# Kernel tuning notes

Measured on AMD Instinct MI355X. Metric: run time of the kernel, lower is better.

The kernel has to match this reference:

```python
import jax, jax.numpy as jnp
import numpy as np

D = 1024; H = 8; QLR = 384; KVLR = 256; NOPE = 128; ROPE = 64; VD = 128
E = 8; TOPK = 2; INTER = 512; NSH = 2; B = 2; T = 2048
QKD = NOPE + ROPE  # 192


def _rms(x, w, eps=1e-6):
    return x * jax.lax.rsqrt(jnp.mean(x * x, axis=-1, keepdims=True) + eps) * w


def _rope(x, cos, sin):
    # x: [B,T,h,ROPE]; pairs are consecutive elements (torch view(...,-1,2)).
    x0 = x[..., 0::2]
    x1 = x[..., 1::2]
    c = cos[None, :, None, :]
    s = sin[None, :, None, :]
    y0 = x0 * c - x1 * s
    y1 = x0 * s + x1 * c
    return jnp.stack([y0, y1], axis=-1).reshape(x.shape)


def setup_inputs() -> dict:
    key = jax.random.key(0)
    ks = jax.random.split(key, 12)
    def w(k, shape, scale=0.02):
        return jax.random.normal(k, shape, dtype=jnp.float32) * scale
    inv = 1.0 / (10000.0 ** (jnp.arange(0, ROPE, 2, dtype=jnp.float32) / ROPE))
    ang = jnp.arange(T, dtype=jnp.float32)[:, None] * inv[None, :]  # [T, ROPE//2]
    return {
        "x": jax.random.normal(ks[0], (B, T, D), dtype=jnp.float32),
        "freqs_cos": jnp.cos(ang),
        "freqs_sin": jnp.sin(ang),
        "rmsn1_w": jnp.ones((D,), jnp.float32),
        "rmsn2_w": jnp.ones((D,), jnp.float32),
        "latent_w": w(ks[1], (D, QLR + KVLR + ROPE)),
        "q_norm_w": jnp.ones((QLR,), jnp.float32),
        "q_up_w": w(ks[2], (QLR, H * QKD)),
        "kv_norm_w": jnp.ones((KVLR,), jnp.float32),
        "kv_up_w": w(ks[3], (KVLR, H * (NOPE + VD))),
        "c_proj_w": w(ks[4], (D, D)),
        "gate_w": w(ks[5], (D, E)),
        "sh_w1": w(ks[6], (D, INTER * NSH)),
        "sh_w2": w(ks[7], (INTER * NSH, D)),
        "sh_w3": w(ks[8], (D, INTER * NSH)),
        "e_w1": w(ks[9], (E, D, INTER)),
        "e_w2": w(ks[10], (E, INTER, D)),
        "e_w3": w(ks[11], (E, D, INTER)),
    }


def reference(x, freqs_cos, freqs_sin, rmsn1_w, rmsn2_w, latent_w, q_norm_w,
              q_up_w, kv_norm_w, kv_up_w, c_proj_w, gate_w, sh_w1, sh_w2,
              sh_w3, e_w1, e_w2, e_w3):
    Bx, Tx, _ = x.shape
    # ---- MLA attention ----
    h = _rms(x, rmsn1_w)
    lat = h @ latent_w
    q_l, kv_l, k_r = jnp.split(lat, [QLR, QLR + KVLR], axis=-1)
    q = (_rms(q_l, q_norm_w) @ q_up_w).reshape(Bx, Tx, H, QKD)
    q_n, q_r = q[..., :NOPE], q[..., NOPE:]
    q_r = _rope(q_r, freqs_cos, freqs_sin)
    q = jnp.concatenate([q_n, q_r], axis=-1)  # [B,T,H,QKD]
    kv = (_rms(kv_l, kv_norm_w) @ kv_up_w).reshape(Bx, Tx, H, NOPE + VD)
    k_n, v = kv[..., :NOPE], kv[..., NOPE:]
    k_r = _rope(k_r[:, :, None, :], freqs_cos, freqs_sin)
    k_r = jnp.broadcast_to(k_r, (Bx, Tx, H, ROPE))
    k = jnp.concatenate([k_n, k_r], axis=-1)
    scale = 1.0 / jnp.sqrt(jnp.float32(QKD))
    scores = jnp.einsum('bqhd,bkhd->bhqk', q, k) * scale
    causal = jnp.tril(jnp.ones((Tx, Tx), dtype=bool))
    scores = jnp.where(causal, scores, jnp.finfo(scores.dtype).min)
    attn = jax.nn.softmax(scores, axis=-1)
    y = jnp.einsum('bhqk,bkhd->bqhd', attn, v).reshape(Bx, Tx, D)
    x = x + y @ c_proj_w
    # ---- DeepSeekMoE ----
    h2 = _rms(x, rmsn2_w).reshape(-1, D)  # [N, D]
    y_sh = (jax.nn.silu(h2 @ sh_w1) * (h2 @ sh_w3)) @ sh_w2
    scores_g = jax.nn.softmax(h2 @ gate_w, axis=-1)  # [N, E]
    w_top, idx = jax.lax.top_k(scores_g, TOPK)  # weights == gathered original scores
    # combine weights per expert (route_scale = 1.0)
    cw = jnp.sum(jax.nn.one_hot(idx, E, dtype=h2.dtype) * w_top[..., None], axis=1)  # [N, E]
    h1 = jnp.einsum('nd,edi->eni', h2, e_w1)
    h3 = jnp.einsum('nd,edi->eni', h2, e_w3)
    out_e = jnp.einsum('eni,eid->end', jax.nn.silu(h1) * h3, e_w2)  # [E, N, D]
    y_moe = y_sh + jnp.einsum('end,ne->nd', out_e, cw)
    return x + y_moe.reshape(Bx, Tx, D)
```

## Files before the change

kernel.cpp:

```cpp
#include <hip/hip_runtime.h>
#include <hip/hip_bf16.h>
#include <math.h>

#define D_ 1024
#define H_ 8
#define QLR_ 384
#define KVLR_ 256
#define NOPE_ 128
#define ROPE_ 64
#define VD_ 128
#define E_ 8
#define INTER_ 512
#define B_ 2
#define T_ 2048
#define QKD_ 192
#define NTOK (B_*T_)
#define LSTR 4608
#define MAXMB 72

typedef __attribute__((ext_vector_type(8))) short short8;
typedef __attribute__((ext_vector_type(4))) float f32x4;
typedef __attribute__((ext_vector_type(4))) unsigned short us4;

__device__ __forceinline__ unsigned short f2bf(float f) {
  union { float f; unsigned u; } v; v.f = f;
  return (unsigned short)((v.u + 0x7FFFu + ((v.u >> 16) & 1u)) >> 16);
}
__device__ __forceinline__ float bf2f(unsigned short h) {
  union { unsigned u; float f; } v; v.u = ((unsigned)h) << 16;
  return v.f;
}

#define GLD16(SRC, DST) __builtin_amdgcn_global_load_lds( \
    (__attribute__((address_space(1))) void*)(SRC), \
    (__attribute__((address_space(3))) void*)(DST), 16, 0, 0)

#define DPPF(v, ctrl) __int_as_float(__builtin_amdgcn_update_dpp(0, __float_as_int(v), ctrl, 0xF, 0xF, true))
__device__ __forceinline__ float dppmax16(float v) {
  v = fmaxf(v, DPPF(v, 0xB1));
  v = fmaxf(v, DPPF(v, 0x4E));
  v = fmaxf(v, DPPF(v, 0x124));
  v = fmaxf(v, DPPF(v, 0x128));
  return v;
}
__device__ __forceinline__ float dppsum16(float v) {
  v += DPPF(v, 0xB1);
  v += DPPF(v, 0x4E);
  v += DPPF(v, 0x124);
  v += DPPF(v, 0x128);
  return v;
}

__global__ __launch_bounds__(256) void transpose_f32_bf16(
    const float* __restrict__ in, unsigned short* __restrict__ out,
    int R, int C, size_t inBS, size_t outBS) {
  __shared__ float tile[32][33];
  const float* inp = in + (size_t)blockIdx.z * inBS;
  unsigned short* outp = out + (size_t)blockIdx.z * outBS;
  int c0 = blockIdx.x * 32, r0 = blockIdx.y * 32;
  int tx = threadIdx.x & 31, ty = threadIdx.x >> 5;
  #pragma unroll
  for (int i = 0; i < 4; ++i) {
    int rr = ty + i * 8;
    tile[rr][tx] = inp[(size_t)(r0 + rr) * C + c0 + tx];
  }
  __syncthreads();
  #pragma unroll
  for (int i = 0; i < 4; ++i) {
    int rr = ty + i * 8;
    outp[(size_t)(c0 + rr) * R + r0 + tx] = f2bf(tile[tx][rr]);
  }
}

__global__ __launch_bounds__(256) void transpose_pair(
    const float* __restrict__ in1, const float* __restrict__ in3,
    unsigned short* __restrict__ out, int K, int C1, size_t inBS, size_t outBS) {
  __shared__ float tile[32][33];
  int z = blockIdx.z; int bat = z >> 1; int f = (z & 1) * 16;
  const float* src = ((z & 1) ? in3 : in1) + (size_t)bat * inBS;
  unsigned short* o = out + (size_t)bat * outBS;
  int c0 = blockIdx.x * 32, r0 = blockIdx.y * 32;
  int tx = threadIdx.x & 31, ty = threadIdx.x >> 5;
  #pragma unroll
  for (int i = 0; i < 4; ++i) {
    int rr = ty + i * 8;
    tile[rr][tx] = src[(size_t)(r0 + rr) * C1 + c0 + tx];
  }
  __syncthreads();
  #pragma unroll
  for (int i = 0; i < 4; ++i) {
    int cc = ty + i * 8;
    int c = c0 + cc;
    int n = ((c >> 4) << 5) + (c & 15) + f;
    o[(size_t)n * K + r0 + tx] = f2bf(tile[tx][cc]);
  }
}

template<typename TI>
__global__ __launch_bounds__(256) void rms_to_bf16(
    const TI* __restrict__ src, int stride, int off, const float* __restrict__ w,
    unsigned short* __restrict__ out, int Dd, int outStride) {
  int row = blockIdx.x;
  const TI* xr = src + (size_t)row * stride + off;
  float ss = 0.f;
  for (int i = threadIdx.x; i < Dd; i += 256) {
    float v;
    if constexpr (sizeof(TI) == 2) v = bf2f((unsigned short)xr[i]); else v = (float)xr[i];
    ss += v * v;
  }
  for (int o = 1; o < 64; o <<= 1) ss += __shfl_xor(ss, o);
  __shared__ float red[4];
  if ((threadIdx.x & 63) == 0) red[threadIdx.x >> 6] = ss;
  __syncthreads();
  float tot = red[0] + red[1] + red[2] + red[3];
  float inv = 1.f / sqrtf(tot / Dd + 1e-6f);
  for (int i = threadIdx.x; i < Dd; i += 256) {
    float v;
    if constexpr (sizeof(TI) == 2) v = bf2f((unsigned short)xr[i]); else v = (float)xr[i];
    out[(size_t)row * outStride + i] = f2bf(v * inv * w[i]);
  }
}

__global__ __launch_bounds__(256) void lat_post(
    const unsigned short* __restrict__ lat, const float* __restrict__ qw,
    const float* __restrict__ kw, const float* __restrict__ fc, const float* __restrict__ fs,
    unsigned short* __restrict__ qn, unsigned short* __restrict__ kvn,
    unsigned short* __restrict__ kr) {
  int row = blockIdx.x, tid = threadIdx.x;
  int lane = tid & 63, wv = tid >> 6;
  const unsigned short* lr = lat + (size_t)row * 768;
  float s1 = 0.f, s2 = 0.f;
  for (int i = tid; i < QLR_; i += 256) { float v = bf2f(lr[i]); s1 += v * v; }
  { float v = bf2f(lr[QLR_ + tid]); s2 = v * v; }
  for (int o = 1; o < 64; o <<= 1) { s1 += __shfl_xor(s1, o); s2 += __shfl_xor(s2, o); }
  __shared__ float red[8];
  if (lane == 0) { red[wv] = s1; red[4 + wv] = s2; }
  __syncthreads();
  float inv1 = 1.f / sqrtf((red[0] + red[1] + red[2] + red[3]) / QLR_ + 1e-6f);
  float inv2 = 1.f / sqrtf((red[4] + red[5] + red[6] + red[7]) / KVLR_ + 1e-6f);
  for (int i = tid; i < QLR_; i += 256)
    qn[(size_t)row * QLR_ + i] = f2bf(bf2f(lr[i]) * inv1 * qw[i]);
  kvn[(size_t)row * KVLR_ + tid] = f2bf(bf2f(lr[QLR_ + tid]) * inv2 * kw[tid]);
  if (tid < 32) {
    int t = row & (T_ - 1);
    float c = fc[t * 32 + tid], s = fs[t * 32 + tid];
    float x0 = bf2f(lr[640 + 2 * tid]), x1 = bf2f(lr[640 + 2 * tid + 1]);
    kr[(size_t)row * ROPE_ + 2 * tid]     = f2bf(x0 * c - x1 * s);
    kr[(size_t)row * ROPE_ + 2 * tid + 1] = f2bf(x0 * s + x1 * c);
  }
}

template<int MODE>
__global__ __launch_bounds__(256) void gemm_bf16(
    const unsigned short* __restrict__ A, const unsigned short* __restrict__ Bt,
    void* __restrict__ Cv, int M, int N, int K,
    const float* __restrict__ addv) {
  __shared__ __align__(16) unsigned short As[128 * 32];
  __shared__ __align__(16) unsigned short Bs[128 * 32];
  const int tid = threadIdx.x;
  const int lane = tid & 63, wave = tid >> 6;
  const int wm = wave >> 1, wn = wave & 1;
  const int bm = blockIdx.y * 128, bn = blockIdx.x * 128;
  const int r = lane & 15, g = lane >> 4;

  f32x4 acc[4][4];
  #pragma unroll
  for (int i = 0; i < 4; ++i)
    #pragma unroll
    for (int j = 0; j < 4; ++j) acc[i][j] = (f32x4)0.f;

  const int rl0 = wave * 16 + (lane >> 2);
  const int rl1 = rl0 + 64;
  const int kc = (lane & 3) * 8;
  char* AsB = (char*)As; char* BsB = (char*)Bs;

  for (int k0 = 0; k0 < K; k0 += 32) {
    GLD16(A + (size_t)(bm + rl0) * K + k0 + kc, AsB + wave * 1024);
    GLD16(A + (size_t)(bm + rl1) * K + k0 + kc, AsB + (wave + 4) * 1024);
    GLD16(Bt + (size_t)(bn + rl0) * K + k0 + kc, BsB + wave * 1024);
    GLD16(Bt + (size_t)(bn + rl1) * K + k0 + kc, BsB + (wave + 4) * 1024);
    __syncthreads();
    short8 af[4], bfr[4];
    #pragma unroll
    for (int mi = 0; mi < 4; ++mi)
      af[mi] = *(const short8*)(As + (wm * 64 + mi * 16 + r) * 32 + g * 8);
    #pragma unroll
    for (int nj = 0; nj < 4; ++nj)
      bfr[nj] = *(const short8*)(Bs + (wn * 64 + nj * 16 + r) * 32 + g * 8);
    #pragma unroll
    for (int mi = 0; mi < 4; ++mi)
      #pragma unroll
      for (int nj = 0; nj < 4; ++nj)
        acc[mi][nj] = __builtin_amdgcn_mfma_f32_16x16x32_bf16(af[mi], bfr[nj], acc[mi][nj], 0, 0, 0);
    __syncthreads();
  }

  const int orow0 = wm * 64 + g * 4;
  const int ocol0 = bn + wn * 64 + r;
  #pragma unroll
  for (int mi = 0; mi < 4; ++mi) {
    #pragma unroll
    for (int reg = 0; reg < 4; ++reg) {
      int mrow = bm + orow0 + mi * 16 + reg;
      size_t bas = (size_t)mrow * N + ocol0;
      if (MODE == 0) {
        unsigned short* C = (unsigned short*)Cv;
        #pragma unroll
        for (int nj = 0; nj < 4; ++nj) C[bas + nj * 16] = f2bf(acc[mi][nj][reg]);
      } else {
        float* C = (float*)Cv;
        #pragma unroll
        for (int nj = 0; nj < 4; ++nj) C[bas + nj * 16] = acc[mi][nj][reg] + addv[bas + nj * 16];
      }
    }
  }
}

__global__ __launch_bounds__(256) void gemm_qkv(
    const unsigned short* __restrict__ qn, const unsigned short* __restrict__ Wqup,
    const unsigned short* __restrict__ kvn, const unsigned short* __restrict__ Wkv,
    unsigned short* __restrict__ qq, unsigned short* __restrict__ kvb,
    unsigned short* __restrict__ vtg) {
  __shared__ __align__(16) unsigned short As[128 * 32];
  __shared__ __align__(16) unsigned short Bs[128 * 32];
  const int tid = threadIdx.x;
  const int lane = tid & 63, wave = tid >> 6;
  const int wm = wave >> 1, wn = wave & 1;
  const bool isQ = blockIdx.x < 12;
  const int bx = isQ ? blockIdx.x : blockIdx.x - 12;
  const unsigned short* A  = isQ ? qn : kvn;
  const unsigned short* Bt = isQ ? Wqup : Wkv;
  const int K = isQ ? QLR_ : KVLR_;
  const int bm = blockIdx.y * 128, bn = bx * 128;
  const int r = lane & 15, g = lane >> 4;

  f32x4 acc[4][4];
  #pragma unroll
  for (int i = 0; i < 4; ++i)
    #pragma unroll
    for (int j = 0; j < 4; ++j) acc[i][j] = (f32x4)0.f;

  const int rl0 = wave * 16 + (lane >> 2);
  const int rl1 = rl0 + 64;
  const int kc = (lane & 3) * 8;
  char* AsB = (char*)As; char* BsB = (char*)Bs;

  for (int k0 = 0; k0 < K; k0 += 32) {
    GLD16(A + (size_t)(bm + rl0) * K + k0 + kc, AsB + wave * 1024);
    GLD16(A + (size_t)(bm + rl1) * K + k0 + kc, AsB + (wave + 4) * 1024);
    GLD16(Bt + (size_t)(bn + rl0) * K + k0 + kc, BsB + wave * 1024);
    GLD16(Bt + (size_t)(bn + rl1) * K + k0 + kc, BsB + (wave + 4) * 1024);
    __syncthreads();
    short8 af[4], bfr[4];
    #pragma unroll
    for (int mi = 0; mi < 4; ++mi)
      af[mi] = *(const short8*)(As + (wm * 64 + mi * 16 + r) * 32 + g * 8);
    #pragma unroll
    for (int nj = 0; nj < 4; ++nj)
      bfr[nj] = *(const short8*)(Bs + (wn * 64 + nj * 16 + r) * 32 + g * 8);
    #pragma unroll
    for (int mi = 0; mi < 4; ++mi)
      #pragma unroll
      for (int nj = 0; nj < 4; ++nj)
        acc[mi][nj] = __builtin_amdgcn_mfma_f32_16x16x32_bf16(af[mi], bfr[nj], acc[mi][nj], 0, 0, 0);
    __syncthreads();
  }

  if (isQ) {
    const int orow0 = wm * 64 + g * 4;
    const int ocol0 = bn + wn * 64 + r;
    #pragma unroll
    for (int mi = 0; mi < 4; ++mi)
      #pragma unroll
      for (int reg = 0; reg < 4; ++reg) {
        int mrow = bm + orow0 + mi * 16 + reg;
        size_t bas = (size_t)mrow * 1536 + ocol0;
        #pragma unroll
        for (int nj = 0; nj < 4; ++nj) qq[bas + nj * 16] = f2bf(acc[mi][nj][reg]);
      }
  } else {
    const int colbase = bn + wn * 64;
    const int b = bm >> 11;
    const int hh = colbase >> 8;
    if ((colbase & 255) < 128) {
      #pragma unroll
      for (int mi = 0; mi < 4; ++mi)
        #pragma unroll
        for (int reg = 0; reg < 4; ++reg) {
          int mrow = bm + wm * 64 + mi * 16 + g * 4 + reg;
          size_t bas = (size_t)mrow * 2048 + colbase + r;
          #pragma unroll
          for (int nj = 0; nj < 4; ++nj) kvb[bas + nj * 16] = f2bf(acc[mi][nj][reg]);
        }
    } else {
      const int tl0 = (bm & 2047) + wm * 64 + g * 4;
      const int d0 = (colbase & 255) - 128 + r;
      const size_t bhbase = (size_t)(b * 8 + hh) * 64;
      #pragma unroll
      for (int mi = 0; mi < 4; ++mi) {
        int t = tl0 + mi * 16;
        size_t tb = (bhbase + (t >> 5)) * 4096 + (t & 31);
        #pragma unroll
        for (int nj = 0; nj < 4; ++nj) {
          int d = d0 + nj * 16;
          us4 pk;
          #pragma unroll
          for (int reg = 0; reg < 4; ++reg) pk[reg] = f2bf(acc[mi][nj][reg]);
          *(us4*)(vtg + tb + (size_t)d * 32) = pk;
        }
      }
    }
  }
}

__global__ __launch_bounds__(256) void gemm_ffn13(
    const unsigned short* __restrict__ h2b, const unsigned short* __restrict__ Wsh13,
    unsigned short* __restrict__ t1m,
    const unsigned short* __restrict__ Wew13, unsigned short* __restrict__ ehm,
    const int* __restrict__ lists, const int* __restrict__ map, const int* __restrict__ sbase) {
  __shared__ __align__(16) unsigned short As[128 * 32];
  __shared__ __align__(16) unsigned short Bs[128 * 32];
  const int i = blockIdx.x;
  const bool isSh = i < 512;
  const int tid = threadIdx.x, lane = tid & 63, wave = tid >> 6;
  const int wm = wave >> 1, wn = wave & 1;
  const int r = lane & 15, g = lane >> 4;
  const int rl0 = wave * 16 + (lane >> 2), rl1 = rl0 + 64;
  const int kc = (lane & 3) * 8;

  int bn, e = 0, ib = 0, bm = 0;
  const unsigned short* Bt;
  int ar0, ar1;
  const unsigned short* A;
  if (isSh) {
    bn = (i & 15) * 128; bm = (i >> 4) * 128;
    Bt = Wsh13; A = h2b;
    ar0 = bm + rl0; ar1 = bm + rl1;
  } else {
    int j = i - 512;
    bn = (j & 7) * 128;
    int mb = map[j >> 3];
    if (mb < 0) return;
    e = mb >> 16; ib = mb & 0xFFFF;
    Bt = Wew13 + (size_t)e * 1024 * 1024; A = h2b;
    ar0 = lists[e * LSTR + ib * 128 + rl0]; if (ar0 < 0) ar0 = 0;
    ar1 = lists[e * LSTR + ib * 128 + rl1]; if (ar1 < 0) ar1 = 0;
  }

  f32x4 acc[4][4];
  #pragma unroll
  for (int a = 0; a < 4; ++a)
    #pragma unroll
    for (int bj = 0; bj < 4; ++bj) acc[a][bj] = (f32x4)0.f;
  char* AsB = (char*)As; char* BsB = (char*)Bs;

  for (int k0 = 0; k0 < 1024; k0 += 32) {
    GLD16(A + (size_t)ar0 * 1024 + k0 + kc, AsB + wave * 1024);
    GLD16(A + (size_t)ar1 * 1024 + k0 + kc, AsB + (wave + 4) * 1024);
    GLD16(Bt + (size_t)(bn + rl0) * 1024 + k0 + kc, BsB + wave * 1024);
    GLD16(Bt + (size_t)(bn + rl1) * 1024 + k0 + kc, BsB + (wave + 4) * 1024);
    __syncthreads();
    short8 af[4], bfr[4];
    #pragma unroll
    for (int mi = 0; mi < 4; ++mi)
      af[mi] = *(const short8*)(As + (wm * 64 + mi * 16 + r) * 32 + g * 8);
    #pragma unroll
    for (int nj = 0; nj < 4; ++nj)
      bfr[nj] = *(const short8*)(Bs + (wn * 64 + nj * 16 + r) * 32 + g * 8);
    #pragma unroll
    for (int mi = 0; mi < 4; ++mi)
      #pragma unroll
      for (int nj = 0; nj < 4; ++nj)
        acc[mi][nj] = __builtin_amdgcn_mfma_f32_16x16x32_bf16(af[mi], bfr[nj], acc[mi][nj], 0, 0, 0);
    __syncthreads();
  }

  if (isSh) {
    const int hc = ((bn + wn * 64) >> 1) + r;
    #pragma unroll
    for (int mi = 0; mi < 4; ++mi)
      #pragma unroll
      for (int reg = 0; reg < 4; ++reg) {
        int mrow = bm + wm * 64 + mi * 16 + g * 4 + reg;
        #pragma unroll
        for (int p = 0; p < 2; ++p) {
          float a = acc[mi][2 * p][reg], b3 = acc[mi][2 * p + 1][reg];
          t1m[(size_t)mrow * 1024 + hc + p * 16] = f2bf((a / (1.f + __expf(-a))) * b3);
        }
      }
  } else {
    const int sb = sbase[e] + ib * 128;
    const int hc = ((bn + wn * 64) >> 1) + r;
    #pragma unroll
    for (int mi = 0; mi < 4; ++mi)
      #pragma unroll
      for (int reg = 0; reg < 4; ++reg) {
        int srow = sb + wm * 64 + mi * 16 + g * 4 + reg;
        #pragma unroll
        for (int p = 0; p < 2; ++p) {
          float a = acc[mi][2 * p][reg], b3 = acc[mi][2 * p + 1][reg];
          ehm[(size_t)srow * 512 + hc + p * 16] = f2bf((a / (1.f + __expf(-a))) * b3);
        }
      }
  }
}

__global__ __launch_bounds__(256) void gemm_ffn2(
    const unsigned short* __restrict__ t1m, const unsigned short* __restrict__ Wsh2,
    const unsigned short* __restrict__ ehm, const unsigned short* __restrict__ Wew2,
    float* __restrict__ out,
    const int* __restrict__ lists, const int* __restrict__ map, const int* __restrict__ sbase,
    const float* __restrict__ cw) {
  __shared__ __align__(16) unsigned short As[128 * 32];
  __shared__ __align__(16) unsigned short Bs[128 * 32];
  const int i = blockIdx.x;
  const bool isSh = i < 256;
  const int tid = threadIdx.x, lane = tid & 63, wave = tid >> 6;
  const int wm = wave >> 1, wn = wave & 1;
  const int r = lane & 15, g = lane >> 4;
  const int rl0 = wave * 16 + (lane >> 2), rl1 = rl0 + 64;
  const int kc = (lane & 3) * 8;

  int bn, e = 0, ib = 0, bm = 0, K;
  const unsigned short* A;
  const unsigned short* Bt;
  if (isSh) {
    bn = (i & 7) * 128; bm = (i >> 3) * 128;
    A = t1m; Bt = Wsh2; K = 1024;
  } else {
    int j = i - 256;
    bn = (j & 7) * 128;
    int mb = map[j >> 3];
    if (mb < 0) return;
    e = mb >> 16; ib = mb & 0xFFFF;
    bm = sbase[e] + ib * 128;
    A = ehm; Bt = Wew2 + (size_t)e * 512 * 1024; K = 512;
  }

  f32x4 acc[4][4];
  #pragma unroll
  for (int a = 0; a < 4; ++a)
    #pragma unroll
    for (int bj = 0; bj < 4; ++bj) acc[a][bj] = (f32x4)0.f;
  char* AsB = (char*)As; char* BsB = (char*)Bs;

  for (int k0 = 0; k0 < K; k0 += 32) {
    GLD16(A + (size_t)(bm + rl0) * K + k0 + kc, AsB + wave * 1024);
    GLD16(A + (size_t)(bm + rl1) * K + k0 + kc, AsB + (wave + 4) * 1024);
    GLD16(Bt + (size_t)(bn + rl0) * K + k0 + kc, BsB + wave * 1024);
    GLD16(Bt + (size_t)(bn + rl1) * K + k0 + kc, BsB + (wave + 4) * 1024);
    __syncthreads();
    short8 af[4], bfr[4];
    #pragma unroll
    for (int mi = 0; mi < 4; ++mi)
      af[mi] = *(const short8*)(As + (wm * 64 + mi * 16 + r) * 32 + g * 8);
    #pragma unroll
    for (int nj = 0; nj < 4; ++nj)
      bfr[nj] = *(const short8*)(Bs + (wn * 64 + nj * 16 + r) * 32 + g * 8);
    #pragma unroll
    for (int mi = 0; mi < 4; ++mi)
      #pragma unroll
      for (int nj = 0; nj < 4; ++nj)
        acc[mi][nj] = __builtin_amdgcn_mfma_f32_16x16x32_bf16(af[mi], bfr[nj], acc[mi][nj], 0, 0, 0);
    __syncthreads();
  }

  const int ocol0 = bn + wn * 64 + r;
  if (isSh) {
    #pragma unroll
    for (int mi = 0; mi < 4; ++mi)
      #pragma unroll
      for (int reg = 0; reg < 4; ++reg) {
        int mrow = bm + wm * 64 + mi * 16 + g * 4 + reg;
        #pragma unroll
        for (int nj = 0; nj < 4; ++nj)
          atomicAdd(out + (size_t)mrow * 1024 + ocol0 + nj * 16, acc[mi][nj][reg]);
      }
  } else {
    #pragma unroll
    for (int mi = 0; mi < 4; ++mi)
      #pragma unroll
      for (int reg = 0; reg < 4; ++reg) {
        int orow = wm * 64 + mi * 16 + g * 4 + reg;
        int tok = lists[e * LSTR + ib * 128 + orow];
        if (tok >= 0) {
          float wt = cw[(size_t)tok * E_ + e];
          #pragma unroll
          for (int nj = 0; nj < 4; ++nj)
            atomicAdd(out + (size_t)tok * 1024 + ocol0 + nj * 16, acc[mi][nj][reg] * wt);
        }
      }
  }
}

#define AQ 128
#define AK 32
#define VP 40
__global__ __launch_bounds__(512) void attn_mfma(
    const unsigned short* __restrict__ q,
    const unsigned short* __restrict__ kv,
    const unsigned short* __restrict__ kr,
    const unsigned short* __restrict__ vt,
    const float* __restrict__ fcos, const float* __restrict__ fsin,
    unsigned short* __restrict__ po,
    float* __restrict__ pml) {
  __shared__ __align__(16) unsigned short Ks[AK * 192];
  __shared__ __align__(16) unsigned short Vl[128 * VP];
  __shared__ __align__(16) unsigned short Ps[8 * 16 * VP];
  const int tid = threadIdx.x, lane = tid & 63, wave = tid >> 6;
  const int r = lane & 15, g = lane >> 4;
  const int bh = blockIdx.y, b = bh >> 3, h = bh & 7;
  const int qt = gridDim.x - 1 - blockIdx.x;
  const int q0 = qt * AQ;
  const int half = blockIdx.z;
  const int hnt = 2 * (qt + 1);
  const int kb = half * hnt, ke = kb + hnt;
  const size_t bT = (size_t)b * T_;
  const unsigned short* vbase = vt + (size_t)bh * 64 * 4096;
  char* KsB = (char*)Ks;

  short8 qf[6];
  const int qrow = q0 + wave * 16 + r;
  {
    const unsigned short* qb = q + ((bT + qrow) * H_ + h) * 192;
    #pragma unroll
    for (int kk = 0; kk < 6; ++kk) qf[kk] = *(const short8*)(qb + kk * 32 + g * 8);
    #pragma unroll
    for (int kk = 4; kk < 6; ++kk) {
      int i0 = (kk - 4) * 16 + g * 4;
      #pragma unroll
      for (int p = 0; p < 4; ++p) {
        float cc = fcos[qrow * 32 + i0 + p], sn = fsin[qrow * 32 + i0 + p];
        float x0 = bf2f((unsigned short)qf[kk][2 * p]), x1 = bf2f((unsigned short)qf[kk][2 * p + 1]);
        qf[kk][2 * p]     = (short)f2bf(x0 * cc - x1 * sn);
        qf[kk][2 * p + 1] = (short)f2bf(x0 * sn + x1 * cc);
      }
    }
  }

  float m_i[4], l_i[4];
  f32x4 o[8];
  #pragma unroll
  for (int i = 0; i < 4; ++i) { m_i[i] = -1e30f; l_i[i] = 0.f; }
  #pragma unroll
  for (int cb = 0; cb < 8; ++cb) o[cb] = (f32x4)0.f;

  const float scale2 = 0.07216878364870322f * 1.44269504088896f;

  const int kr0r = tid / 24, kr0c = tid % 24;
  const bool k1v = tid < 256;
  const int kr1r = (tid + 512) / 24, kr1c = (tid + 512) % 24;

  short8 kreg0, kreg1, vreg;
  {
    int kk0 = kb * AK;
    kreg0 = (kr0c < 16)
      ? *(const short8*)(kv + ((bT + kk0 + kr0r) * H_ + h) * 256 + kr0c * 8)
      : *(const short8*)(kr + (bT + kk0 + kr0r) * 64 + (kr0c - 16) * 8);
    if (k1v)
      kreg1 = (kr1c < 16)
        ? *(const short8*)(kv + ((bT + kk0 + kr1r) * H_ + h) * 256 + kr1c * 8)
        : *(const short8*)(kr + (bT + kk0 + kr1r) * 64 + (kr1c - 16) * 8);
    vreg = *(const short8*)(vbase + (size_t)kb * 4096 + tid * 8);
  }

  for (int kt = kb; kt < ke; ++kt) {
    __builtin_amdgcn_s_barrier();
    __builtin_amdgcn_sched_barrier(0);
    *(short8*)(KsB + ((kr0r * 384 + kr0c * 16) ^ ((kr0r & 7) << 4))) = kreg0;
    if (k1v)
      *(short8*)(KsB + ((kr1r * 384 + kr1c * 16) ^ ((kr1r & 7) << 4))) = kreg1;
    *(short8*)(Vl + (tid >> 2) * VP + (tid & 3) * 8) = vreg;
    asm volatile("s_waitcnt lgkmcnt(0)" ::: "memory");
    __builtin_amdgcn_s_barrier();
    __builtin_amdgcn_sched_barrier(0);

    if (kt + 1 < ke) {
      int k1 = (kt + 1) * AK;
      kreg0 = (kr0c < 16)
        ? *(const short8*)(kv + ((bT + k1 + kr0r) * H_ + h) * 256 + kr0c * 8)
        : *(const short8*)(kr + (bT + k1 + kr0r) * 64 + (kr0c - 16) * 8);
      if (k1v)
        kreg1 = (kr1c < 16)
          ? *(const short8*)(kv + ((bT + k1 + kr1r) * H_ + h) * 256 + kr1c * 8)
          : *(const short8*)(kr + (bT + k1 + kr1r) * 64 + (kr1c - 16) * 8);
      vreg = *(const short8*)(vbase + (size_t)(kt + 1) * 4096 + tid * 8);
    }

    const int k0 = kt * AK;
    f32x4 sf0 = (f32x4)0.f, sf1 = (f32x4)0.f;
    {
      int ksw = (r & 7) << 4;
      __builtin_amdgcn_s_setprio(1);
      #pragma unroll
      for (int kk = 0; kk < 6; ++kk) {
        short8 b0 = *(const short8*)(KsB + ((r * 384 + kk * 64 + g * 16) ^ ksw));
        short8 b1 = *(const short8*)(KsB + (((16 + r) * 384 + kk * 64 + g * 16) ^ ksw));
        sf0 = __builtin_amdgcn_mfma_f32_16x16x32_bf16(qf[kk], b0, sf0, 0, 0, 0);
        sf1 = __builtin_amdgcn_mfma_f32_16x16x32_bf16(qf[kk], b1, sf1, 0, 0, 0);
      }
      __builtin_amdgcn_s_setprio(0);
    }

    float fac[4];
    bool needs = false;
    const bool bnd = (k0 + AK > q0);
    #pragma unroll
    for (int reg = 0; reg < 4; ++reg) {
      float s0 = sf0[reg] * scale2;
      float s1 = sf1[reg] * scale2;
      if (bnd) {
        int qp = q0 + wave * 16 + g * 4 + reg;
        if (k0 + r > qp) s0 = -1e30f;
        if (k0 + 16 + r > qp) s1 = -1e30f;
      }
      float mt = dppmax16(fmaxf(s0, s1));
      float fc = 1.f, mn = m_i[reg];
      if (mt > mn + 8.f) {
        mn = mt; fc = exp2f(m_i[reg] - mn); m_i[reg] = mn; needs = true;
      }
      float e0 = exp2f(s0 - mn), e1 = exp2f(s1 - mn);
      float rs = dppsum16(e0 + e1);
      l_i[reg] = l_i[reg] * fc + rs;
      fac[reg] = fc;
      __hip_bfloat162 pk = __float22bfloat162_rn(float2{e0, e1});
      unsigned u = *(unsigned*)&pk;
      int prow = g * 4 + reg;
      Ps[wave * 16 * VP + prow * VP + r] = (unsigned short)u;
      Ps[wave * 16 * VP + prow * VP + 16 + r] = (unsigned short)(u >> 16);
    }
    if (__any(needs)) {
      #pragma unroll
      for (int cb = 0; cb < 8; ++cb)
        #pragma unroll
        for (int reg = 0; reg < 4; ++reg) o[cb][reg] *= fac[reg];
    }
    short8 pa = *(const short8*)(Ps + wave * 16 * VP + r * VP + g * 8);
    __builtin_amdgcn_s_setprio(1);
    #pragma unroll
    for (int cb = 0; cb < 8; ++cb) {
      short8 vb = *(const short8*)(Vl + (cb * 16 + r) * VP + g * 8);
      o[cb] = __builtin_amdgcn_mfma_f32_16x16x32_bf16(pa, vb, o[cb], 0, 0, 0);
    }
    __builtin_amdgcn_s_setprio(0);
  }

  const int slab = (bh * 16 + qt) * 2 + half;
  unsigned short* pob = po + (size_t)slab * 16384;
  float* pmlb = pml + (size_t)slab * 256;
  #pragma unroll
  for (int reg = 0; reg < 4; ++reg) {
    int row = wave * 16 + g * 4 + reg;
    if (r == 0) { pmlb[row * 2] = m_i[reg]; pmlb[row * 2 + 1] = l_i[reg]; }
    #pragma unroll
    for (int cb = 0; cb < 8; ++cb)
      pob[row * 128 + cb * 16 + r] = f2bf(o[cb][reg]);
  }
}

__global__ __launch_bounds__(512) void attn_combine(
    const unsigned short* __restrict__ po, const float* __restrict__ pml,
    unsigned short* __restrict__ y) {
  const int qt = blockIdx.x, bh = blockIdx.y, b = bh >> 3, h = bh & 7;
  const int s0 = (bh * 16 + qt) * 2, s1 = s0 + 1;
  const int row = threadIdx.x >> 2;
  const int qp = threadIdx.x & 3;
  float m0 = pml[(size_t)s0 * 256 + row * 2], l0 = pml[(size_t)s0 * 256 + row * 2 + 1];
  float m1 = pml[(size_t)s1 * 256 + row * 2], l1 = pml[(size_t)s1 * 256 + row * 2 + 1];
  float m = fmaxf(m0, m1);
  float e0 = exp2f(m0 - m), e1 = exp2f(m1 - m);
  float inv = 1.f / (l0 * e0 + l1 * e1);
  e0 *= inv; e1 *= inv;
  const unsigned short* o0 = po + (size_t)s0 * 16384 + row * 128 + qp * 32;
  const unsigned short* o1 = po + (size_t)s1 * 16384 + row * 128 + qp * 32;
  unsigned short* yb = y + ((size_t)(b * T_ + qt * 128 + row)) * 1024 + h * 128 + qp * 32;
  #pragma unroll
  for (int v = 0; v < 4; ++v) {
    short8 a = *(const short8*)(o0 + v * 8);
    short8 c = *(const short8*)(o1 + v * 8);
    short8 w;
    #pragma unroll
    for (int j = 0; j < 8; ++j)
      w[j] = (short)f2bf(bf2f((unsigned short)a[j]) * e0 + bf2f((unsigned short)c[j]) * e1);
    *(short8*)(yb + v * 8) = w;
  }
}

__global__ __launch_bounds__(256) void rms2_gate(
    const float* __restrict__ xo, const float* __restrict__ rw, const float* __restrict__ gw,
    unsigned short* __restrict__ h2b, float* __restrict__ cw) {
  int row = blockIdx.x, tid = threadIdx.x;
  int lane = tid & 63, wv = tid >> 6;
  const float* xr = xo + (size_t)row * D_;
  float v[4]; float ss = 0.f;
  #pragma unroll
  for (int j = 0; j < 4; ++j) { v[j] = xr[tid + j * 256]; ss += v[j] * v[j]; }
  for (int o = 1; o < 64; o <<= 1) ss += __shfl_xor(ss, o);
  __shared__ float red[4];
  if (lane == 0) red[wv] = ss;
  __syncthreads();
  float inv = 1.f / sqrtf((red[0] + red[1] + red[2] + red[3]) / D_ + 1e-6f);
  float a[E_] = {0, 0, 0, 0, 0, 0, 0, 0};
  #pragma unroll
  for (int j = 0; j < 4; ++j) {
    int i = tid + j * 256;
    float hv = v[j] * inv * rw[i];
    h2b[(size_t)row * D_ + i] = f2bf(hv);
    const float* wr = gw + (size_t)i * E_;
    #pragma unroll
    for (int e = 0; e < E_; ++e) a[e] += hv * wr[e];
  }
  #pragma unroll
  for (int e = 0; e < E_; ++e) {
    float t = a[e];
    for (int o = 1; o < 64; o <<= 1) t += __shfl_xor(t, o);
    a[e] = t;
  }
  __shared__ float ga[4][E_];
  if (lane == 0)
    #pragma unroll
    for (int e = 0; e < E_; ++e) ga[wv][e] = a[e];
  __syncthreads();
  if (tid == 0) {
    float lg[E_];
    #pragma unroll
    for (int e = 0; e < E_; ++e) lg[e] = ga[0][e] + ga[1][e] + ga[2][e] + ga[3][e];
    float mx = lg[0];
    #pragma unroll
    for (int e = 1; e < E_; ++e) mx = fmaxf(mx, lg[e]);
    float sum = 0.f; float p[E_];
    #pragma unroll
    for (int e = 0; e < E_; ++e) { p[e] = __expf(lg[e] - mx); sum += p[e]; }
    float is = 1.f / sum;
    int i1 = 0; float b1 = p[0];
    #pragma unroll
    for (int e = 1; e < E_; ++e) if (p[e] > b1) { b1 = p[e]; i1 = e; }
    int i2 = -1; float b2 = -1.f;
    #pragma unroll
    for (int e = 0; e < E_; ++e) if (e != i1 && p[e] > b2) { b2 = p[e]; i2 = e; }
    #pragma unroll
    for (int e = 0; e < E_; ++e)
      cw[(size_t)row * E_ + e] = (e == i1) ? b1 * is : (e == i2 ? b2 * is : 0.f);
  }
}

__global__ __launch_bounds__(256) void moe_build(const float* __restrict__ cw,
                                                 int* __restrict__ lists, int* __restrict__ counts) {
  int e = blockIdx.x, tid = threadIdx.x;
  int lane = tid & 63, wv = tid >> 6;
  __shared__ int wsum[4];
  __shared__ int base;
  if (tid == 0) base = 0;
  __syncthreads();
  for (int c0 = 0; c0 < NTOK; c0 += 256) {
    int tok = c0 + tid;
    bool f = cw[(size_t)tok * E_ + e] > 0.f;
    unsigned long long m = __ballot(f);
    int pos = __popcll(m & ((1ull << lane) - 1ull));
    if (lane == 0) wsum[wv] = __popcll(m);
    __syncthreads();
    int woff = base;
    #pragma unroll
    for (int w = 0; w < 4; ++w) if (w < wv) woff += wsum[w];
    if (f) lists[e * LSTR + woff + pos] = tok;
    __syncthreads();
    if (tid == 0) base += wsum[0] + wsum[1] + wsum[2] + wsum[3];
    __syncthreads();
  }
  int cnt = base;
  int padded = (cnt + 127) & ~127;
  for (int i2 = cnt + tid; i2 < padded; i2 += 256) lists[e * LSTR + i2] = -1;
  if (tid == 0) { counts[e] = cnt; counts[8 + e] = padded >> 7; }
}

__global__ void moe_finalize(const int* __restrict__ counts, int* __restrict__ map,
                             int* __restrict__ sbase) {
  if (threadIdx.x == 0 && blockIdx.x == 0) {
    int cum = 0;
    for (int e = 0; e < E_; ++e) {
      sbase[e] = cum * 128;
      int nb = counts[8 + e];
      for (int i = 0; i < nb; ++i) map[cum + i] = (e << 16) | i;
      cum += nb;
    }
    for (; cum < MAXMB; ++cum) map[cum] = -1;
  }
}

extern "C" void kernel_launch(void* const* d_in, const int* in_sizes, int n_in,
                              void* d_out, int out_size, void* d_ws, size_t ws_size,
                              hipStream_t stream) {
  const float* x        = (const float*)d_in[0];
  const float* fcos     = (const float*)d_in[1];
  const float* fsin     = (const float*)d_in[2];
  const float* rmsn1_w  = (const float*)d_in[3];
  const float* rmsn2_w  = (const float*)d_in[4];
  const float* latent_w = (const float*)d_in[5];
  const float* q_norm_w = (const float*)d_in[6];
  const float* q_up_w   = (const float*)d_in[7];
  const float* kv_norm_w= (const float*)d_in[8];
  const float* kv_up_w  = (const float*)d_in[9];
  const float* c_proj_w = (const float*)d_in[10];
  const float* gate_w   = (const float*)d_in[11];
  const float* sh_w1    = (const float*)d_in[12];
  const float* sh_w2    = (const float*)d_in[13];
  const float* sh_w3    = (const float*)d_in[14];
  const float* e_w1     = (const float*)d_in[15];
  const float* e_w2     = (const float*)d_in[16];
  const float* e_w3     = (const float*)d_in[17];
  float* out = (float*)d_out;

  char* base = (char*)d_ws;
  size_t off = 0;
  auto take = [&](size_t bytes) { char* p = base + off; off += (bytes + 255) & ~(size_t)255; return p; };
  unsigned short* Wlat  = (unsigned short*)take((size_t)768 * 1024 * 2);
  unsigned short* Wqup  = (unsigned short*)take((size_t)1536 * 384 * 2);
  unsigned short* Wkv   = (unsigned short*)take((size_t)2048 * 256 * 2);
  unsigned short* Wcp   = (unsigned short*)take((size_t)1024 * 1024 * 2);
  unsigned short* Wsh13 = (unsigned short*)take((size_t)2048 * 1024 * 2);
  unsigned short* Wsh2  = (unsigned short*)take((size_t)1024 * 1024 * 2);
  unsigned short* Wew13 = (unsigned short*)take((size_t)8 * 1024 * 1024 * 2);
  unsigned short* Wew2  = (unsigned short*)take((size_t)8 * 1024 * 512 * 2);
  float* cw             = (float*)take((size_t)NTOK * E_ * 4);
  int* lists            = (int*)take((size_t)E_ * LSTR * 4);
  int* counts           = (int*)take(64 * 4);
  int* map              = (int*)take(MAXMB * 4);
  int* sbase            = (int*)take(E_ * 4);
  unsigned short* Vtg   = (unsigned short*)take((size_t)16 * 64 * 4096 * 2);
  unsigned short* kr    = (unsigned short*)take((size_t)NTOK * 64 * 2);
  float* pml            = (float*)take((size_t)512 * 256 * 4);

  size_t actStart = off;
  size_t aoff = actStart;
  auto takeA = [&](size_t bytes) { char* p = base + aoff; aoff += (bytes + 255) & ~(size_t)255; return p; };
  unsigned short* h_bf = (unsigned short*)takeA((size_t)NTOK * 1024 * 2);
  unsigned short* lat  = (unsigned short*)takeA((size_t)NTOK * 768 * 2);
  unsigned short* qn   = (unsigned short*)takeA((size_t)NTOK * 384 * 2);
  unsigned short* kvn  = (unsigned short*)takeA((size_t)NTOK * 256 * 2);
  unsigned short* qq   = (unsigned short*)takeA((size_t)NTOK * 1536 * 2);
  unsigned short* kvb  = (unsigned short*)takeA((size_t)NTOK * 2048 * 2);
  unsigned short* y    = (unsigned short*)takeA((size_t)NTOK * 1024 * 2);

  unsigned short* po   = (unsigned short*)(base + actStart);

  size_t coff = actStart;
  auto takeC = [&](size_t bytes) { char* p = base + coff; coff += (bytes + 255) & ~(size_t)255; return p; };
  unsigned short* h2b  = (unsigned short*)takeC((size_t)NTOK * 1024 * 2);
  unsigned short* t1m  = (unsigned short*)takeC((size_t)NTOK * 1024 * 2);
  unsigned short* ehm  = (unsigned short*)takeC((size_t)9216 * 512 * 2);

  dim3 blk(256);

  transpose_f32_bf16<<<dim3(22, 32, 1), blk, 0, stream>>>(latent_w, Wlat, 1024, 704, 0, 0);
  transpose_f32_bf16<<<dim3(48, 12, 1), blk, 0, stream>>>(q_up_w, Wqup, 384, 1536, 0, 0);
  transpose_f32_bf16<<<dim3(64, 8, 1), blk, 0, stream>>>(kv_up_w, Wkv, 256, 2048, 0, 0);
  transpose_f32_bf16<<<dim3(32, 32, 1), blk, 0, stream>>>(c_proj_w, Wcp, 1024, 1024, 0, 0);
  transpose_f32_bf16<<<dim3(32, 32, 1), blk, 0, stream>>>(sh_w2, Wsh2, 1024, 1024, 0, 0);
  transpose_pair<<<dim3(32, 32, 2), blk, 0, stream>>>(sh_w1, sh_w3, Wsh13, 1024, 1024, 0, 0);
  transpose_pair<<<dim3(16, 32, 16), blk, 0, stream>>>(e_w1, e_w3, Wew13, 1024, 512,
      (size_t)1024 * 512, (size_t)1024 * 1024);
  transpose_f32_bf16<<<dim3(32, 16, 8), blk, 0, stream>>>(e_w2, Wew2, 512, 1024,
      (size_t)512 * 1024, (size_t)1024 * 512);

  rms_to_bf16<float><<<NTOK, blk, 0, stream>>>(x, D_, 0, rmsn1_w, h_bf, D_, D_);
  gemm_bf16<0><<<dim3(6, 32), blk, 0, stream>>>(h_bf, Wlat, lat, NTOK, 768, 1024, nullptr);
  lat_post<<<NTOK, blk, 0, stream>>>(lat, q_norm_w, kv_norm_w, fcos, fsin, qn, kvn, kr);
  gemm_qkv<<<dim3(28, 32), blk, 0, stream>>>(qn, Wqup, kvn, Wkv, qq, kvb, Vtg);
  attn_mfma<<<dim3(T_ / AQ, B_ * H_, 2), dim3(512), 0, stream>>>(qq, kvb, kr, Vtg, fcos, fsin, po, pml);
  attn_combine<<<dim3(T_ / AQ, B_ * H_), dim3(512), 0, stream>>>(po, pml, y);
  gemm_bf16<1><<<dim3(8, 32), blk, 0, stream>>>(y, Wcp, out, NTOK, 1024, 1024, x);
  rms2_gate<<<NTOK, blk, 0, stream>>>(out, rmsn2_w, gate_w, h2b, cw);
  moe_build<<<E_, blk, 0, stream>>>(cw, lists, counts);
  moe_finalize<<<1, 64, 0, stream>>>(counts, map, sbase);
  gemm_ffn13<<<dim3(1088), blk, 0, stream>>>(h2b, Wsh13, t1m, Wew13, ehm, lists, map, sbase);
  gemm_ffn2<<<dim3(832), blk, 0, stream>>>(t1m, Wsh2, ehm, Wew2, out, lists, map, sbase, cw);
}
```

Measured before the change: 388.8 us.

## Merge weight transposes, RMSNorm and latent GEMM into two combined launches

Replaces the eight weight-transpose launches, the RMSNorm launch and the latent GEMM launch with two heterogeneous kernels. prep1 runs the first RMSNorm alongside the latent_w transpose, and prep2 runs the latent GEMM alongside all the other weight transposes, dispatching on block index. The aim is to cut launch overhead and let small kernels overlap with one another. In exchange, the GEMM blocks now carry the extra shared-memory footprint of the transpose tile, which may lower occupancy, and they all share one launch configuration.

Result: faster. 359.7 us (-7.5%).

```diff
diff --git a/kernel.cpp b/kernel.cpp
--- a/kernel.cpp
+++ b/kernel.cpp
@@ -51,35 +51,23 @@
   return v;
 }
 
-__global__ __launch_bounds__(256) void transpose_f32_bf16(
-    const float* __restrict__ in, unsigned short* __restrict__ out,
-    int R, int C, size_t inBS, size_t outBS) {
-  __shared__ float tile[32][33];
-  const float* inp = in + (size_t)blockIdx.z * inBS;
-  unsigned short* outp = out + (size_t)blockIdx.z * outBS;
-  int c0 = blockIdx.x * 32, r0 = blockIdx.y * 32;
+__device__ __forceinline__ void trans32(const float* __restrict__ src, unsigned short* __restrict__ dst,
+                                        int R, int C, int c0, int r0, float (*tile)[33]) {
   int tx = threadIdx.x & 31, ty = threadIdx.x >> 5;
   #pragma unroll
   for (int i = 0; i < 4; ++i) {
     int rr = ty + i * 8;
-    tile[rr][tx] = inp[(size_t)(r0 + rr) * C + c0 + tx];
+    tile[rr][tx] = src[(size_t)(r0 + rr) * C + c0 + tx];
   }
   __syncthreads();
   #pragma unroll
   for (int i = 0; i < 4; ++i) {
     int rr = ty + i * 8;
-    outp[(size_t)(c0 + rr) * R + r0 + tx] = f2bf(tile[tx][rr]);
-  }
-}
-
-__global__ __launch_bounds__(256) void transpose_pair(
-    const float* __restrict__ in1, const float* __restrict__ in3,
-    unsigned short* __restrict__ out, int K, int C1, size_t inBS, size_t outBS) {
-  __shared__ float tile[32][33];
-  int z = blockIdx.z; int bat = z >> 1; int f = (z & 1) * 16;
-  const float* src = ((z & 1) ? in3 : in1) + (size_t)bat * inBS;
-  unsigned short* o = out + (size_t)bat * outBS;
-  int c0 = blockIdx.x * 32, r0 = blockIdx.y * 32;
+    dst[(size_t)(c0 + rr) * R + r0 + tx] = f2bf(tile[tx][rr]);
+  }
+}
+__device__ __forceinline__ void trans32p(const float* __restrict__ src, unsigned short* __restrict__ dst,
+                                         int K, int C1, int c0, int r0, int f, float (*tile)[33]) {
   int tx = threadIdx.x & 31, ty = threadIdx.x >> 5;
   #pragma unroll
   for (int i = 0; i < 4; ++i) {
@@ -92,32 +80,123 @@
     int cc = ty + i * 8;
     int c = c0 + cc;
     int n = ((c >> 4) << 5) + (c & 15) + f;
-    o[(size_t)n * K + r0 + tx] = f2bf(tile[tx][cc]);
-  }
-}
-
-template<typename TI>
-__global__ __launch_bounds__(256) void rms_to_bf16(
-    const TI* __restrict__ src, int stride, int off, const float* __restrict__ w,
-    unsigned short* __restrict__ out, int Dd, int outStride) {
-  int row = blockIdx.x;
-  const TI* xr = src + (size_t)row * stride + off;
-  float ss = 0.f;
-  for (int i = threadIdx.x; i < Dd; i += 256) {
-    float v;
-    if constexpr (sizeof(TI) == 2) v = bf2f((unsigned short)xr[i]); else v = (float)xr[i];
-    ss += v * v;
-  }
-  for (int o = 1; o < 64; o <<= 1) ss += __shfl_xor(ss, o);
-  __shared__ float red[4];
-  if ((threadIdx.x & 63) == 0) red[threadIdx.x >> 6] = ss;
-  __syncthreads();
-  float tot = red[0] + red[1] + red[2] + red[3];
-  float inv = 1.f / sqrtf(tot / Dd + 1e-6f);
-  for (int i = threadIdx.x; i < Dd; i += 256) {
-    float v;
-    if constexpr (sizeof(TI) == 2) v = bf2f((unsigned short)xr[i]); else v = (float)xr[i];
-    out[(size_t)row * outStride + i] = f2bf(v * inv * w[i]);
+    dst[(size_t)n * K + r0 + tx] = f2bf(tile[tx][cc]);
+  }
+}
+
+__global__ __launch_bounds__(256) void prep1(
+    const float* __restrict__ x, const float* __restrict__ rw, unsigned short* __restrict__ h_bf,
+    const float* __restrict__ latent_w, unsigned short* __restrict__ Wlat) {
+  __shared__ float tile[32][33];
+  int b = blockIdx.x;
+  if (b < NTOK) {
+    int tid = threadIdx.x;
+    const float* xr = x + (size_t)b * D_;
+    float v[4]; float ss = 0.f;
+    #pragma unroll
+    for (int j = 0; j < 4; ++j) { v[j] = xr[tid + j * 256]; ss += v[j] * v[j]; }
+    for (int o = 1; o < 64; o <<= 1) ss += __shfl_xor(ss, o);
+    if ((tid & 63) == 0) tile[32][tid >> 6] = ss;
+    __syncthreads();
+    float inv = 1.f / sqrtf((tile[32][0] + tile[32][1] + tile[32][2] + tile[32][3]) / D_ + 1e-6f);
+    #pragma unroll
+    for (int j = 0; j < 4; ++j) {
+      int i = tid + j * 256;
+      h_bf[(size_t)b * D_ + i] = f2bf(v[j] * inv * rw[i]);
+    }
+    return;
+  }
+  b -= NTOK;
+  trans32(latent_w, Wlat, 1024, 704, (b % 22) * 32, (b / 22) * 32, tile);
+}
+
+__global__ __launch_bounds__(256) void prep2(
+    const unsigned short* __restrict__ h_bf, const unsigned short* __restrict__ Wlat,
+    unsigned short* __restrict__ lat,
+    const float* __restrict__ q_up_w, unsigned short* __restrict__ Wqup,
+    const float* __restrict__ kv_up_w, unsigned short* __restrict__ Wkv,
+    const float* __restrict__ c_proj_w, unsigned short* __restrict__ Wcp,
+    const float* __restrict__ sh_w1, const float* __restrict__ sh_w3, unsigned short* __restrict__ Wsh13,
+    const float* __restrict__ sh_w2, unsigned short* __restrict__ Wsh2,
+    const float* __restrict__ e_w1, const float* __restrict__ e_w3, unsigned short* __restrict__ Wew13,
+    const float* __restrict__ e_w2, unsigned short* __restrict__ Wew2) {
+  __shared__ __align__(16) unsigned short As[128 * 32];
+  __shared__ __align__(16) unsigned short Bs[128 * 32];
+  __shared__ float tile[32][33];
+  int b = blockIdx.x;
+  if (b < 192) {
+    const int tid = threadIdx.x, lane = tid & 63, wave = tid >> 6;
+    const int wm = wave >> 1, wn = wave & 1;
+    const int bm = (b / 6) * 128, bn = (b % 6) * 128;
+    const int r = lane & 15, g = lane >> 4;
+    f32x4 acc[4][4];
+    #pragma unroll
+    for (int i = 0; i < 4; ++i)
+      #pragma unroll
+      for (int j = 0; j < 4; ++j) acc[i][j] = (f32x4)0.f;
+    const int rl0 = wave * 16 + (lane >> 2), rl1 = rl0 + 64;
+    const int kc = (lane & 3) * 8;
+    char* AsB = (char*)As; char* BsB = (char*)Bs;
+    for (int k0 = 0; k0 < 1024; k0 += 32) {
+      GLD16(h_bf + (size_t)(bm + rl0) * 1024 + k0 + kc, AsB + wave * 1024);
+      GLD16(h_bf + (size_t)(bm + rl1) * 1024 + k0 + kc, AsB + (wave + 4) * 1024);
+      GLD16(Wlat + (size_t)(bn + rl0) * 1024 + k0 + kc, BsB + wave * 1024);
+      GLD16(Wlat + (size_t)(bn + rl1) * 1024 + k0 + kc, BsB + (wave + 4) * 1024);
+      __syncthreads();
+      short8 af[4], bfr[4];
+      #pragma unroll
+      for (int mi = 0; mi < 4; ++mi)
+        af[mi] = *(const short8*)(As + (wm * 64 + mi * 16 + r) * 32 + g * 8);
+      #pragma unroll
+      for (int nj = 0; nj < 4; ++nj)
+        bfr[nj] = *(const short8*)(Bs + (wn * 64 + nj * 16 + r) * 32 + g * 8);
+      #pragma unroll
+      for (int mi = 0; mi < 4; ++mi)
+        #pragma unroll
+        for (int nj = 0; nj < 4; ++nj)
+          acc[mi][nj] = __builtin_amdgcn_mfma_f32_16x16x32_bf16(af[mi], bfr[nj], acc[mi][nj], 0, 0, 0);
+      __syncthreads();
+    }
+    const int orow0 = wm * 64 + g * 4;
+    const int ocol0 = bn + wn * 64 + r;
+    #pragma unroll
+    for (int mi = 0; mi < 4; ++mi)
+      #pragma unroll
+      for (int reg = 0; reg < 4; ++reg) {
+        int mrow = bm + orow0 + mi * 16 + reg;
+        size_t bas = (size_t)mrow * 768 + ocol0;
+        #pragma unroll
+        for (int nj = 0; nj < 4; ++nj) lat[bas + nj * 16] = f2bf(acc[mi][nj][reg]);
+      }
+    return;
+  }
+  b -= 192;
+  if (b < 576) { trans32(q_up_w, Wqup, 384, 1536, (b % 48) * 32, (b / 48) * 32, tile); return; }
+  b -= 576;
+  if (b < 512) { trans32(kv_up_w, Wkv, 256, 2048, (b % 64) * 32, (b / 64) * 32, tile); return; }
+  b -= 512;
+  if (b < 1024) { trans32(c_proj_w, Wcp, 1024, 1024, (b % 32) * 32, (b / 32) * 32, tile); return; }
+  b -= 1024;
+  if (b < 1024) { trans32(sh_w2, Wsh2, 1024, 1024, (b % 32) * 32, (b / 32) * 32, tile); return; }
+  b -= 1024;
+  if (b < 2048) {
+    int z = b / 1024, idx = b % 1024;
+    trans32p(z ? sh_w3 : sh_w1, Wsh13, 1024, 1024, (idx % 32) * 32, (idx / 32) * 32, z * 16, tile);
+    return;
+  }
+  b -= 2048;
+  if (b < 8192) {
+    int z = b / 512, idx = b % 512;
+    int bat = z >> 1, f = (z & 1) * 16;
+    const float* src = ((z & 1) ? e_w3 : e_w1) + (size_t)bat * 1024 * 512;
+    trans32p(src, Wew13 + (size_t)bat * 1024 * 1024, 1024, 512, (idx % 16) * 32, (idx / 16) * 32, f, tile);
+    return;
+  }
+  b -= 8192;
+  {
+    int z = b / 512, idx = b % 512;
+    trans32(e_w2 + (size_t)z * 512 * 1024, Wew2 + (size_t)z * 1024 * 512,
+            512, 1024, (idx % 32) * 32, (idx / 32) * 32, tile);
   }
 }
 
@@ -851,19 +930,10 @@
 
   dim3 blk(256);
 
-  transpose_f32_bf16<<<dim3(22, 32, 1), blk, 0, stream>>>(latent_w, Wlat, 1024, 704, 0, 0);
-  transpose_f32_bf16<<<dim3(48, 12, 1), blk, 0, stream>>>(q_up_w, Wqup, 384, 1536, 0, 0);
-  transpose_f32_bf16<<<dim3(64, 8, 1), blk, 0, stream>>>(kv_up_w, Wkv, 256, 2048, 0, 0);
-  transpose_f32_bf16<<<dim3(32, 32, 1), blk, 0, stream>>>(c_proj_w, Wcp, 1024, 1024, 0, 0);
-  transpose_f32_bf16<<<dim3(32, 32, 1), blk, 0, stream>>>(sh_w2, Wsh2, 1024, 1024, 0, 0);
-  transpose_pair<<<dim3(32, 32, 2), blk, 0, stream>>>(sh_w1, sh_w3, Wsh13, 1024, 1024, 0, 0);
-  transpose_pair<<<dim3(16, 32, 16), blk, 0, stream>>>(e_w1, e_w3, Wew13, 1024, 512,
-      (size_t)1024 * 512, (size_t)1024 * 1024);
-  transpose_f32_bf16<<<dim3(32, 16, 8), blk, 0, stream>>>(e_w2, Wew2, 512, 1024,
-      (size_t)512 * 1024, (size_t)1024 * 512);
-
-  rms_to_bf16<float><<<NTOK, blk, 0, stream>>>(x, D_, 0, rmsn1_w, h_bf, D_, D_);
-  gemm_bf16<0><<<dim3(6, 32), blk, 0, stream>>>(h_bf, Wlat, lat, NTOK, 768, 1024, nullptr);
+  prep1<<<dim3(NTOK + 704), blk, 0, stream>>>(x, rmsn1_w, h_bf, latent_w, Wlat);
+  prep2<<<dim3(192 + 576 + 512 + 1024 + 1024 + 2048 + 8192 + 4096), blk, 0, stream>>>(
+      h_bf, Wlat, lat, q_up_w, Wqup, kv_up_w, Wkv, c_proj_w, Wcp,
+      sh_w1, sh_w3, Wsh13, sh_w2, Wsh2, e_w1, e_w3, Wew13, e_w2, Wew2);
   lat_post<<<NTOK, blk, 0, stream>>>(lat, q_norm_w, kv_norm_w, fcos, fsin, qn, kvn, kr);
   gemm_qkv<<<dim3(28, 32), blk, 0, stream>>>(qn, Wqup, kvn, Wkv, qq, kvb, Vtg);
   attn_mfma<<<dim3(T_ / AQ, B_ * H_, 2), dim3(512), 0, stream>>>(qq, kvb, kr, Vtg, fcos, fsin, po, pml);
```
